# Optimization experiments

Hardware: AMD Instinct MI355X
Metric: run time of the kernel (lower is better)

## Reference

```python
import jax, jax.numpy as jnp
import numpy as np

N, E, IN_D, H, OUT_D = 50000, 800000, 128, 64, 64


def setup_inputs() -> dict:
    key = jax.random.key(0)
    ks = jax.random.split(key, 16)
    s = lambda k, shape: jax.random.normal(k, shape, dtype=jnp.float32) * (1.0 / np.sqrt(shape[0]))
    return {
        "x": jax.random.normal(ks[0], (N, IN_D), dtype=jnp.float32),
        "edge_index": jax.random.randint(ks[1], (2, E), 0, N, dtype=jnp.int32),
        "W1": s(ks[2], (IN_D, H)), "b1": jnp.zeros((H,), jnp.float32),
        "W2": s(ks[3], (H, 2 * H)), "b2": jnp.zeros((2 * H,), jnp.float32),
        "W3": s(ks[4], (2 * H, 4 * H)), "b3": jnp.zeros((4 * H,), jnp.float32),
        "dec1_w": s(ks[5], (4 * H, 2 * H, 2)), "dec1_b": jnp.zeros((2 * H,), jnp.float32),
        "dec2_w": s(ks[6], (2 * H, H, 2)), "dec2_b": jnp.zeros((H,), jnp.float32),
        "dec3_w": s(ks[7], (H, H, 2)), "dec3_b": jnp.zeros((H,), jnp.float32),
        "skip1_w": s(ks[8], (2 * H, 2 * H)), "skip1_b": jnp.zeros((2 * H,), jnp.float32),
        "skip2_w": s(ks[9], (H, H)), "skip2_b": jnp.zeros((H,), jnp.float32),
        "fin_w": s(ks[10], (OUT_D, 8 * H)), "fin_b": jnp.zeros((OUT_D,), jnp.float32),
    }


def _deconv2(x, w, b):
    # ConvTranspose1d(kernel=2, stride=2): [n,c,l] x [c,o,2] -> [n,o,2l]
    y = jnp.einsum('ncl,cok->nolk', x, w)
    n, o = x.shape[0], w.shape[1]
    return y.reshape(n, o, -1) + b[None, :, None]


def reference(x, edge_index, W1, b1, W2, b2, W3, b3, dec1_w, dec1_b, dec2_w, dec2_b,
              dec3_w, dec3_b, skip1_w, skip1_b, skip2_w, skip2_b, fin_w, fin_b):
    n = x.shape[0]
    loop = jnp.arange(n, dtype=edge_index.dtype)
    src = jnp.concatenate([edge_index[0], loop])
    tgt = jnp.concatenate([edge_index[1], loop])
    deg = jax.ops.segment_sum(jnp.ones_like(src, dtype=x.dtype), tgt, num_segments=n)
    dinv = jax.lax.rsqrt(deg)  # deg >= 1 due to self-loops
    norm = dinv[src] * dinv[tgt]  # [E+N]

    def gcn(h, W, b):
        hw = h @ W
        agg = jax.ops.segment_sum(hw[src] * norm[:, None], tgt, num_segments=n)
        return agg + b

    x1 = jax.nn.gelu(gcn(x, W1, b1))    # [N, H]
    x2 = jax.nn.gelu(gcn(x1, W2, b2))   # [N, 2H]
    x3 = jax.nn.gelu(gcn(x2, W3, b3))   # [N, 4H]

    d = _deconv2(x3[:, :, None], dec1_w, dec1_b)           # [N, 2H, 2]
    d = d + (x2 @ skip1_w.T + skip1_b)[:, :, None]
    d = _deconv2(d, dec2_w, dec2_b)                        # [N, H, 4]
    d = d + (x1 @ skip2_w.T + skip2_b)[:, :, None]
    d = _deconv2(d, dec3_w, dec3_b)                        # [N, H, 8]
    out = d.reshape(n, -1) @ fin_w.T + fin_b               # [N, OUT_D]
    return out
```

## Files before the change

### kernel.cpp

```cpp
#include <hip/hip_runtime.h>
#include <hip/hip_bf16.h>

typedef __attribute__((ext_vector_type(8))) short short8_t;
typedef __attribute__((ext_vector_type(4))) float f32x4;

#define CAP 64

__device__ __forceinline__ float gelu_f(float x) {
    float x3 = x * x * x;
    return 0.5f * x * (1.0f + tanhf(0.7978845608028654f * (x + 0.044715f * x3)));
}
__device__ __forceinline__ float b2f(unsigned short u) {
    union { float f; unsigned int i; } c; c.i = ((unsigned int)u) << 16; return c.f;
}
__device__ __forceinline__ unsigned short f2bu(float f) {
    union { float f; unsigned int i; } c; c.f = f;
    unsigned int r = c.i + 0x7fffu + ((c.i >> 16) & 1u);
    return (unsigned short)(r >> 16);
}


__device__ __forceinline__ void d_EF(int bid, int t, const float* __restrict__ dec3_w,
                                     const float* __restrict__ fin_w, float* __restrict__ EF) {
    int i2 = bid * 4 + (t >> 6), od = t & 63;
    int c3 = i2 >> 2, pp = i2 & 3;
    const float* d3 = dec3_w + c3 * 128;
    const float* fw = fin_w + od * 512;
    float s = 0.f;
    #pragma unroll
    for (int o3 = 0; o3 < 64; ++o3) {
        s += d3[o3 * 2 + 0] * fw[o3 * 8 + pp * 2 + 0];
        s += d3[o3 * 2 + 1] * fw[o3 * 8 + pp * 2 + 1];
    }
    EF[i2 * 64 + od] = s;
}

__device__ __forceinline__ void d_CEF(int bid, int t, const float* __restrict__ dec2_w,
                                      const float* __restrict__ EF, float* __restrict__ CEF) {
    int i1 = bid * 4 + (t >> 6), od = t & 63;
    int c2 = i1 >> 1, lp = i1 & 1;
    const float* d2 = dec2_w + c2 * 128;
    float s = 0.f;
    #pragma unroll
    for (int o2 = 0; o2 < 64; ++o2) {
        s += d2[o2 * 2 + 0] * EF[(o2 * 4 + lp * 2 + 0) * 64 + od];
        s += d2[o2 * 2 + 1] * EF[(o2 * 4 + lp * 2 + 1) * 64 + od];
    }
    CEF[i1 * 64 + od] = s;
}

__device__ __forceinline__ void d_comp(int sb, int od,
                       const float* __restrict__ dec1_w, const float* __restrict__ skip1_w,
                       const float* __restrict__ skip2_w,
                       const float* __restrict__ dec1_b, const float* __restrict__ skip1_b,
                       const float* __restrict__ dec2_b, const float* __restrict__ skip2_b,
                       const float* __restrict__ dec3_b, const float* __restrict__ fin_w,
                       const float* __restrict__ fin_b,
                       const float* __restrict__ CEF, const float* __restrict__ EF,
                       unsigned short* __restrict__ McatT, float* __restrict__ m0) {
    if (sb < 256) {
        const float* d1 = dec1_w + sb * 256;
        float s = 0.f;
        for (int j = 0; j < 256; ++j) s += d1[j] * CEF[j * 64 + od];
        McatT[od * 448 + sb] = f2bu(s);
    } else if (sb < 384) {
        int c = sb - 256;
        float s = 0.f;
        for (int j = 0; j < 256; ++j) s += skip1_w[(j >> 1) * 128 + c] * CEF[j * 64 + od];
        McatT[od * 448 + sb] = f2bu(s);
    } else if (sb < 448) {
        int c = sb - 384;
        float s = 0.f;
        for (int j = 0; j < 256; ++j) s += skip2_w[(j >> 2) * 64 + c] * EF[j * 64 + od];
        McatT[od * 448 + sb] = f2bu(s);
    } else {
        float s = fin_b[od];
        for (int j = 0; j < 256; ++j) s += (dec1_b[j >> 1] + skip1_b[j >> 1]) * CEF[j * 64 + od];
        for (int j = 0; j < 256; ++j) s += (dec2_b[j >> 2] + skip2_b[j >> 2]) * EF[j * 64 + od];
        for (int j = 0; j < 512; ++j) s += dec3_b[j >> 3] * fin_w[od * 512 + j];
        m0[od] = s;
    }
}

__device__ __forceinline__ void d_wconv(int bid, int t,
                        const float* __restrict__ W1, const float* __restrict__ W2,
                        const float* __restrict__ W3,
                        unsigned short* __restrict__ W1T, unsigned short* __restrict__ W2T,
                        unsigned short* __restrict__ W3T) {
    int i = bid * 256 + t;
    if (i < 8192) {
        int k = i >> 6, n = i & 63;
        W1T[n * 128 + k] = f2bu(W1[i]);
    } else if (i < 16384) {
        int j = i - 8192; int k = j >> 7, n = j & 127;
        W2T[n * 64 + k] = f2bu(W2[j]);
    } else if (i < 49152) {
        int j = i - 16384; int k = j >> 8, n = j & 255;
        W3T[n * 128 + k] = f2bu(W3[j]);
    }
}

__device__ __forceinline__ void d_fillx(int bid, int t, const int* __restrict__ src,
                                        const int* __restrict__ tgt, int E,
                                        int* __restrict__ cnt, int* __restrict__ csr) {
    int i = (bid * 256 + t) * 8;
    if (i + 7 < E) {
        int4 t0 = *(const int4*)(tgt + i);
        int4 t1 = *(const int4*)(tgt + i + 4);
        int4 s0 = *(const int4*)(src + i);
        int4 s1 = *(const int4*)(src + i + 4);
        int k0 = atomicAdd(&cnt[t0.x], 1);
        int k1 = atomicAdd(&cnt[t0.y], 1);
        int k2 = atomicAdd(&cnt[t0.z], 1);
        int k3 = atomicAdd(&cnt[t0.w], 1);
        int k4 = atomicAdd(&cnt[t1.x], 1);
        int k5 = atomicAdd(&cnt[t1.y], 1);
        int k6 = atomicAdd(&cnt[t1.z], 1);
        int k7 = atomicAdd(&cnt[t1.w], 1);
        if (k0 < CAP) csr[(t0.x << 6) + k0] = s0.x;
        if (k1 < CAP) csr[(t0.y << 6) + k1] = s0.y;
        if (k2 < CAP) csr[(t0.z << 6) + k2] = s0.z;
        if (k3 < CAP) csr[(t0.w << 6) + k3] = s0.w;
        if (k4 < CAP) csr[(t1.x << 6) + k4] = s1.x;
        if (k5 < CAP) csr[(t1.y << 6) + k5] = s1.y;
        if (k6 < CAP) csr[(t1.z << 6) + k6] = s1.z;
        if (k7 < CAP) csr[(t1.w << 6) + k7] = s1.w;
    } else {
        for (int k = i; k < E; ++k) {
            int tt = tgt[k];
            int kk = atomicAdd(&cnt[tt], 1);
            if (kk < CAP) csr[(tt << 6) + kk] = src[k];
        }
    }
}

template<bool A32, bool BIAS, bool GELU, bool OUT32>
__device__ __forceinline__ void d_gmm(
    int bx, int by,
    const unsigned short* __restrict__ A, const float* __restrict__ Af, int lda,
    const unsigned short* __restrict__ Bt,
    const float* __restrict__ bias,
    void* __restrict__ Cv, int ldc, int M, int K) {
    constexpr int LDS_R = 72;
    __shared__ unsigned short As[64 * LDS_R];
    __shared__ unsigned short Bs[64 * LDS_R];
    const int tid = threadIdx.x;
    const int r0 = bx * 64, c0 = by * 64;
    const int w = tid >> 6, lane = tid & 63;
    const int wm = (w >> 1) * 32, wn = (w & 1) * 32;
    const int fr = lane & 15, kg = lane >> 4;
    f32x4 acc[2][2];
    #pragma unroll
    for (int m = 0; m < 2; ++m)
        #pragma unroll
        for (int n = 0; n < 2; ++n) { f32x4 z = {0.f, 0.f, 0.f, 0.f}; acc[m][n] = z; }

    const int sr = tid >> 2, sc = (tid & 3) * 16;
    const bool aok = (r0 + sr) < M;
    const unsigned short* ag = A32 ? nullptr : (A + (size_t)(r0 + sr) * lda + sc);
    const float* agf = A32 ? (Af + (size_t)(r0 + sr) * lda + sc) : nullptr;
    const unsigned short* bg = Bt + (size_t)(c0 + sr) * K + sc;

    for (int kt = 0; kt < K; kt += 64) {
        if (aok) {
            if constexpr (A32) {
                float4 f0 = *(const float4*)(agf + kt);
                float4 f1 = *(const float4*)(agf + kt + 4);
                float4 f2 = *(const float4*)(agf + kt + 8);
                float4 f3 = *(const float4*)(agf + kt + 12);
                unsigned short o[16] = { f2bu(f0.x), f2bu(f0.y), f2bu(f0.z), f2bu(f0.w),
                                         f2bu(f1.x), f2bu(f1.y), f2bu(f1.z), f2bu(f1.w),
                                         f2bu(f2.x), f2bu(f2.y), f2bu(f2.z), f2bu(f2.w),
                                         f2bu(f3.x), f2bu(f3.y), f2bu(f3.z), f2bu(f3.w) };
                *(uint4*)&As[sr * LDS_R + sc]     = ((const uint4*)o)[0];
                *(uint4*)&As[sr * LDS_R + sc + 8] = ((const uint4*)o)[1];
            } else {
                *(uint4*)&As[sr * LDS_R + sc]     = *(const uint4*)(ag + kt);
                *(uint4*)&As[sr * LDS_R + sc + 8] = *(const uint4*)(ag + kt + 8);
            }
        }
        *(uint4*)&Bs[sr * LDS_R + sc]     = *(const uint4*)(bg + kt);
        *(uint4*)&Bs[sr * LDS_R + sc + 8] = *(const uint4*)(bg + kt + 8);
        __syncthreads();
        #pragma unroll
        for (int s2 = 0; s2 < 2; ++s2) {
            short8_t afr[2], bfr[2];
            #pragma unroll
            for (int n = 0; n < 2; ++n)
                bfr[n] = *(const short8_t*)&Bs[(wn + n * 16 + fr) * LDS_R + s2 * 32 + kg * 8];
            #pragma unroll
            for (int m = 0; m < 2; ++m)
                afr[m] = *(const short8_t*)&As[(wm + m * 16 + fr) * LDS_R + s2 * 32 + kg * 8];
            #pragma unroll
            for (int m = 0; m < 2; ++m)
                #pragma unroll
                for (int n = 0; n < 2; ++n)
                    acc[m][n] = __builtin_amdgcn_mfma_f32_16x16x32_bf16(afr[m], bfr[n], acc[m][n], 0, 0, 0);
        }
        __syncthreads();
    }
    #pragma unroll
    for (int m = 0; m < 2; ++m) {
        #pragma unroll
        for (int n = 0; n < 2; ++n) {
            #pragma unroll
            for (int j = 0; j < 4; ++j) {
                int row = r0 + wm + m * 16 + kg * 4 + j;
                int col = c0 + wn + n * 16 + fr;
                if (row < M) {
                    float xv = acc[m][n][j];
                    if (BIAS) xv += bias[col];
                    if (GELU) xv = gelu_f(xv);
                    if (OUT32) ((float*)Cv)[(size_t)row * ldc + col] = xv;
                    else ((unsigned short*)Cv)[(size_t)row * ldc + col] = f2bu(xv);
                }
            }
        }
    }
}

template<int F, int LPN, bool EPI>
__device__ __forceinline__ void d_aggb(
    int bid,
    const unsigned short* __restrict__ g, int ldi,
    const int* __restrict__ cnt, const int* __restrict__ csr,
    const float* __restrict__ bias,
    unsigned short* __restrict__ out, int ldo, int N) {
    constexpr int SLOTS = 64 / LPN;
    static_assert(F / LPN == 8, "V must be 8");
    __shared__ int   sIdx[4][CAP];
    __shared__ float sW[4][CAP];
    int tid = threadIdx.x;
    int lane = tid & 63, wv = tid >> 6;
    int v = bid * 4 + wv;
    bool ok = v < N;
    int vc = ok ? v : 0;
    int slot = lane / LPN, fl = lane % LPN;
    int fo = fl * 8;
    int deg = cnt[vc];
    float dv = rsqrtf((float)(deg + 1));
    int degc = min(deg, CAP);
    int u_l = (lane < degc) ? csr[(vc << 6) + lane] : vc;
    sIdx[wv][lane] = u_l;
    sW[wv][lane] = rsqrtf((float)(cnt[u_l] + 1)) * dv;
    __syncthreads();
    if (!ok) return;
    int cntE = degc + 1;
    float acc[8] = {};
    const unsigned short* hbase = g + fo;
    int j = slot;
    for (; j + SLOTS < cntE; j += 2 * SLOTS) {
        int s0 = (j > 0) ? (j - 1) : 0;
        int u0 = (j == 0) ? v : sIdx[wv][s0];
        float w0 = (j == 0) ? dv * dv : sW[wv][s0];
        int u1 = sIdx[wv][j + SLOTS - 1];
        float w1 = sW[wv][j + SLOTS - 1];
        uint4 t0 = *(const uint4*)(hbase + (size_t)u0 * ldi);
        uint4 t1 = *(const uint4*)(hbase + (size_t)u1 * ldi);
        const unsigned short* a0 = (const unsigned short*)&t0;
        const unsigned short* a1 = (const unsigned short*)&t1;
        #pragma unroll
        for (int q = 0; q < 8; ++q) acc[q] = fmaf(b2f(a0[q]), w0, acc[q]);
        #pragma unroll
        for (int q = 0; q < 8; ++q) acc[q] = fmaf(b2f(a1[q]), w1, acc[q]);
    }
    if (j < cntE) {
        int s0 = (j > 0) ? (j - 1) : 0;
        int u = (j == 0) ? v : sIdx[wv][s0];
        float wgt = (j == 0) ? dv * dv : sW[wv][s0];
        uint4 t = *(const uint4*)(hbase + (size_t)u * ldi);
        const unsigned short* ts = (const unsigned short*)&t;
        #pragma unroll
        for (int q = 0; q < 8; ++q) acc[q] = fmaf(b2f(ts[q]), wgt, acc[q]);
    }
    #pragma unroll
    for (int off = LPN; off < 64; off <<= 1)
        #pragma unroll
        for (int q = 0; q < 8; ++q) acc[q] += __shfl_xor(acc[q], off, 64);
    if (slot == 0) {
        unsigned short o[8];
        #pragma unroll
        for (int q = 0; q < 8; ++q) {
            float xv = acc[q];
            if (EPI) xv = gelu_f(xv + bias[fo + q]);
            o[q] = f2bu(xv);
        }
        *(uint4*)(out + (size_t)v * ldo + fo) = *(const uint4*)o;
    }
}


template<bool A32, bool BIAS, bool GELU, bool OUT32>
__global__ __launch_bounds__(256) void k_gmm(
    const unsigned short* __restrict__ A, const float* __restrict__ Af, int lda,
    const unsigned short* __restrict__ Bt,
    const float* __restrict__ bias,
    void* __restrict__ Cv, int ldc, int M, int K) {
    d_gmm<A32, BIAS, GELU, OUT32>(blockIdx.x, blockIdx.y, A, Af, lda, Bt, bias, Cv, ldc, M, K);
}

template<int F, int LPN, bool EPI>
__global__ __launch_bounds__(256) void k_aggb(
    const unsigned short* __restrict__ g, int ldi,
    const int* __restrict__ cnt, const int* __restrict__ csr,
    const float* __restrict__ bias,
    unsigned short* __restrict__ out, int ldo, int N) {
    d_aggb<F, LPN, EPI>(blockIdx.x, g, ldi, cnt, csr, bias, out, ldo, N);
}

__global__ __launch_bounds__(256) void k_mega0(
    const float* __restrict__ W1, const float* __restrict__ W2, const float* __restrict__ W3,
    unsigned short* __restrict__ W1T, unsigned short* __restrict__ W2T,
    unsigned short* __restrict__ W3T,
    const float* __restrict__ dec3_w, const float* __restrict__ fin_w, float* __restrict__ EF,
    int* __restrict__ cnt, int N) {
    int b = blockIdx.x, t = threadIdx.x;
    if (b < 192) d_wconv(b, t, W1, W2, W3, W1T, W2T, W3T);
    else if (b < 256) d_EF(b - 192, t, dec3_w, fin_w, EF);
    else { int i = (b - 256) * 256 + t; if (i < N) cnt[i] = 0; }
}

__global__ __launch_bounds__(256) void k_megaA(
    const int* __restrict__ src, const int* __restrict__ tgt, int E,
    int* __restrict__ cnt, int* __restrict__ csr, int nf,
    const float* __restrict__ x, const unsigned short* __restrict__ W1T,
    unsigned short* __restrict__ hw1, int M, int ng,
    const float* __restrict__ dec2_w, const float* __restrict__ EF, float* __restrict__ CEF) {
    int b = blockIdx.x;
    if (b < nf)
        d_fillx(b, threadIdx.x, src, tgt, E, cnt, csr);
    else if (b < nf + ng)
        d_gmm<true, false, false, false>(b - nf, 0, nullptr, x, 128, W1T,
                                         (const float*)nullptr, hw1, 64, M, 128);
    else
        d_CEF(b - nf - ng, threadIdx.x, dec2_w, EF, CEF);
}

__global__ __launch_bounds__(256) void k_megaB(
    const unsigned short* __restrict__ hw1,
    const int* __restrict__ cnt, const int* __restrict__ csr,
    const float* __restrict__ b1, unsigned short* __restrict__ x1out, int N, int na,
    const float* __restrict__ dec1_w, const float* __restrict__ skip1_w,
    const float* __restrict__ skip2_w,
    const float* __restrict__ dec1_b, const float* __restrict__ skip1_b,
    const float* __restrict__ dec2_b, const float* __restrict__ skip2_b,
    const float* __restrict__ dec3_b, const float* __restrict__ fin_w,
    const float* __restrict__ fin_b,
    const float* __restrict__ CEF, const float* __restrict__ EF,
    unsigned short* __restrict__ McatT, float* __restrict__ m0) {
    int b = blockIdx.x, t = threadIdx.x;
    if (b < na) {
        d_aggb<64, 8, true>(b, hw1, 64, cnt, csr, b1, x1out, 448, N);
    } else {
        int sb = (b - na) * 4 + (t >> 6);
        if (sb <= 448)
            d_comp(sb, t & 63, dec1_w, skip1_w, skip2_w, dec1_b, skip1_b, dec2_b, skip2_b,
                   dec3_b, fin_w, fin_b, CEF, EF, McatT, m0);
    }
}

extern "C" void kernel_launch(void* const* d_in, const int* in_sizes, int n_in,
                              void* d_out, int out_size, void* d_ws, size_t ws_size,
                              hipStream_t stream) {
    const float* x       = (const float*)d_in[0];
    const int*   ei      = (const int*)d_in[1];
    const float* W1      = (const float*)d_in[2];
    const float* b1      = (const float*)d_in[3];
    const float* W2      = (const float*)d_in[4];
    const float* b2      = (const float*)d_in[5];
    const float* W3      = (const float*)d_in[6];
    const float* b3      = (const float*)d_in[7];
    const float* dec1_w  = (const float*)d_in[8];
    const float* dec1_b  = (const float*)d_in[9];
    const float* dec2_w  = (const float*)d_in[10];
    const float* dec2_b  = (const float*)d_in[11];
    const float* dec3_w  = (const float*)d_in[12];
    const float* dec3_b  = (const float*)d_in[13];
    const float* skip1_w = (const float*)d_in[14];
    const float* skip1_b = (const float*)d_in[15];
    const float* skip2_w = (const float*)d_in[16];
    const float* skip2_b = (const float*)d_in[17];
    const float* fin_w   = (const float*)d_in[18];
    const float* fin_b   = (const float*)d_in[19];

    const int N = in_sizes[0] / 128;
    const int E = in_sizes[1] / 2;
    const int* e_src = ei;
    const int* e_tgt = ei + E;

    char* p = (char*)d_ws;
    auto alloc = [&](size_t bytes) -> void* {
        void* r = p;
        p += (bytes + 255) & ~(size_t)255;
        return r;
    };
    int*   cnt     = (int*)alloc((size_t)N * 4);
    int*   csr     = (int*)alloc((size_t)N * CAP * 4);
    float* EF      = (float*)alloc(256 * 64 * 4);
    float* CEF     = (float*)alloc(256 * 64 * 4);
    float* m0      = (float*)alloc(64 * 4);
    unsigned short* McatT = (unsigned short*)alloc(64 * 448 * 2);
    unsigned short* W1T   = (unsigned short*)alloc(64 * 128 * 2);
    unsigned short* W2T   = (unsigned short*)alloc(128 * 64 * 2);
    unsigned short* W3T   = (unsigned short*)alloc(256 * 128 * 2);
    unsigned short* hw1   = (unsigned short*)alloc((size_t)N * 64 * 2);
    unsigned short* a1    = (unsigned short*)alloc((size_t)N * 64 * 2);
    unsigned short* xcat  = (unsigned short*)alloc((size_t)N * 448 * 2);
    unsigned short* a2    = hw1;
    if ((size_t)(p - (char*)d_ws) > ws_size) return;

    const int nf = (E / 8 + 255) / 256;
    const int mg = (N + 63) / 64;
    const int ag = (N + 3) / 4;
    const int compb = (449 + 3) / 4;
    const int zb = (N + 255) / 256;

    k_mega0<<<dim3(192 + 64 + zb), dim3(256), 0, stream>>>(
        W1, W2, W3, W1T, W2T, W3T, dec3_w, fin_w, EF, cnt, N);

    k_megaA<<<dim3(nf + mg + 64), dim3(256), 0, stream>>>(
        e_src, e_tgt, E, cnt, csr, nf, x, W1T, hw1, N, mg, dec2_w, EF, CEF);

    k_megaB<<<dim3(ag + compb), dim3(256), 0, stream>>>(
        hw1, cnt, csr, b1, xcat + 384, N, ag,
        dec1_w, skip1_w, skip2_w, dec1_b, skip1_b, dec2_b, skip2_b, dec3_b,
        fin_w, fin_b, CEF, EF, McatT, m0);

    k_aggb<64, 8, false><<<dim3(ag), dim3(256), 0, stream>>>(
        xcat + 384, 448, cnt, csr, (const float*)nullptr, a1, 64, N);
    k_gmm<false, true, true, false><<<dim3(mg, 2), dim3(256), 0, stream>>>(
        a1, nullptr, 64, W2T, b2, xcat + 256, 448, N, 64);

    k_aggb<128, 16, false><<<dim3(ag), dim3(256), 0, stream>>>(
        xcat + 256, 448, cnt, csr, (const float*)nullptr, a2, 128, N);
    k_gmm<false, true, true, false><<<dim3(mg, 4), dim3(256), 0, stream>>>(
        a2, nullptr, 128, W3T, b3, xcat, 448, N, 128);

    k_gmm<false, true, false, true><<<dim3(mg, 1), dim3(256), 0, stream>>>(
        xcat, nullptr, 448, McatT, m0, d_out, 64, N, 448);
}
```

Before: 213.9 us.

## Process two nodes per wavefront in GCN aggregation to raise memory parallelism

Each wavefront in the neighbor-aggregation routine now handles two destination nodes, interleaving four independent row gathers per iteration instead of two. The self-loop is folded into the shared-memory neighbor list, with zero-weight padding beyond the degree, which removes per-iteration branching. The intent is more gathers in flight per wave and half as many blocks. In exchange it uses more registers, does wasted zero-weight loads when the two nodes have unequal degrees, and lowers the neighbor cap by one.

New measurement: 203.3 us. 5.0% less time.

```diff
diff --git a/kernel.cpp b/kernel.cpp
--- a/kernel.cpp
+++ b/kernel.cpp
@@ -228,64 +228,94 @@
     unsigned short* __restrict__ out, int ldo, int N) {
     constexpr int SLOTS = 64 / LPN;
     static_assert(F / LPN == 8, "V must be 8");
-    __shared__ int   sIdx[4][CAP];
-    __shared__ float sW[4][CAP];
+    __shared__ int   sIdx[4][2][CAP];
+    __shared__ float sW[4][2][CAP];
     int tid = threadIdx.x;
     int lane = tid & 63, wv = tid >> 6;
-    int v = bid * 4 + wv;
-    bool ok = v < N;
-    int vc = ok ? v : 0;
+    int v0 = bid * 8 + wv * 2;
+    int v1 = v0 + 1;
+    bool ok0 = v0 < N, ok1 = v1 < N;
+    int vc0 = ok0 ? v0 : 0, vc1 = ok1 ? v1 : 0;
     int slot = lane / LPN, fl = lane % LPN;
     int fo = fl * 8;
-    int deg = cnt[vc];
-    float dv = rsqrtf((float)(deg + 1));
-    int degc = min(deg, CAP);
-    int u_l = (lane < degc) ? csr[(vc << 6) + lane] : vc;
-    sIdx[wv][lane] = u_l;
-    sW[wv][lane] = rsqrtf((float)(cnt[u_l] + 1)) * dv;
+    int deg0 = cnt[vc0], deg1 = cnt[vc1];
+    float dv0 = rsqrtf((float)(deg0 + 1)), dv1 = rsqrtf((float)(deg1 + 1));
+    int degc0 = min(deg0, CAP - 1), degc1 = min(deg1, CAP - 1);
+    int ua = (lane < degc0) ? csr[(vc0 << 6) + lane] : vc0;
+    int ub = (lane < degc1) ? csr[(vc1 << 6) + lane] : vc1;
+    int ca = cnt[ua], cb = cnt[ub];
+    float wa = (lane < degc0) ? rsqrtf((float)(ca + 1)) * dv0
+                              : ((lane == degc0) ? dv0 * dv0 : 0.f);
+    float wb = (lane < degc1) ? rsqrtf((float)(cb + 1)) * dv1
+                              : ((lane == degc1) ? dv1 * dv1 : 0.f);
+    sIdx[wv][0][lane] = ua;  sW[wv][0][lane] = wa;
+    sIdx[wv][1][lane] = ub;  sW[wv][1][lane] = wb;
     __syncthreads();
-    if (!ok) return;
-    int cntE = degc + 1;
-    float acc[8] = {};
+    int cntE0 = ok0 ? degc0 + 1 : 0;
+    int cntE1 = ok1 ? degc1 + 1 : 0;
+    int cmax = max(cntE0, cntE1);
+    float acc0[8] = {}, acc1[8] = {};
     const unsigned short* hbase = g + fo;
     int j = slot;
-    for (; j + SLOTS < cntE; j += 2 * SLOTS) {
-        int s0 = (j > 0) ? (j - 1) : 0;
-        int u0 = (j == 0) ? v : sIdx[wv][s0];
-        float w0 = (j == 0) ? dv * dv : sW[wv][s0];
-        int u1 = sIdx[wv][j + SLOTS - 1];
-        float w1 = sW[wv][j + SLOTS - 1];
+    for (; j + SLOTS < cmax; j += 2 * SLOTS) {
+        int u00 = sIdx[wv][0][j];          float w00 = sW[wv][0][j];
+        int u01 = sIdx[wv][0][j + SLOTS];  float w01 = sW[wv][0][j + SLOTS];
+        int u10 = sIdx[wv][1][j];          float w10 = sW[wv][1][j];
+        int u11 = sIdx[wv][1][j + SLOTS];  float w11 = sW[wv][1][j + SLOTS];
+        uint4 t00 = *(const uint4*)(hbase + (size_t)u00 * ldi);
+        uint4 t01 = *(const uint4*)(hbase + (size_t)u01 * ldi);
+        uint4 t10 = *(const uint4*)(hbase + (size_t)u10 * ldi);
+        uint4 t11 = *(const uint4*)(hbase + (size_t)u11 * ldi);
+        const unsigned short* p00 = (const unsigned short*)&t00;
+        const unsigned short* p01 = (const unsigned short*)&t01;
+        const unsigned short* p10 = (const unsigned short*)&t10;
+        const unsigned short* p11 = (const unsigned short*)&t11;
+        #pragma unroll
+        for (int q = 0; q < 8; ++q) {
+            acc0[q] = fmaf(b2f(p00[q]), w00, acc0[q]);
+            acc1[q] = fmaf(b2f(p10[q]), w10, acc1[q]);
+        }
+        #pragma unroll
+        for (int q = 0; q < 8; ++q) {
+            acc0[q] = fmaf(b2f(p01[q]), w01, acc0[q]);
+            acc1[q] = fmaf(b2f(p11[q]), w11, acc1[q]);
+        }
+    }
+    if (j < cmax) {
+        int u0 = sIdx[wv][0][j];  float w0 = sW[wv][0][j];
+        int u1 = sIdx[wv][1][j];  float w1 = sW[wv][1][j];
         uint4 t0 = *(const uint4*)(hbase + (size_t)u0 * ldi);
         uint4 t1 = *(const uint4*)(hbase + (size_t)u1 * ldi);
-        const unsigned short* a0 = (const unsigned short*)&t0;
-        const unsigned short* a1 = (const unsigned short*)&t1;
-        #pragma unroll
-        for (int q = 0; q < 8; ++q) acc[q] = fmaf(b2f(a0[q]), w0, acc[q]);
-        #pragma unroll
-        for (int q = 0; q < 8; ++q) acc[q] = fmaf(b2f(a1[q]), w1, acc[q]);
-    }
-    if (j < cntE) {
-        int s0 = (j > 0) ? (j - 1) : 0;
-        int u = (j == 0) ? v : sIdx[wv][s0];
-        float wgt = (j == 0) ? dv * dv : sW[wv][s0];
-        uint4 t = *(const uint4*)(hbase + (size_t)u * ldi);
-        const unsigned short* ts = (const unsigned short*)&t;
-        #pragma unroll
-        for (int q = 0; q < 8; ++q) acc[q] = fmaf(b2f(ts[q]), wgt, acc[q]);
+        const unsigned short* p0 = (const unsigned short*)&t0;
+        const unsigned short* p1 = (const unsigned short*)&t1;
+        #pragma unroll
+        for (int q = 0; q < 8; ++q) {
+            acc0[q] = fmaf(b2f(p0[q]), w0, acc0[q]);
+            acc1[q] = fmaf(b2f(p1[q]), w1, acc1[q]);
+        }
     }
     #pragma unroll
     for (int off = LPN; off < 64; off <<= 1)
         #pragma unroll
-        for (int q = 0; q < 8; ++q) acc[q] += __shfl_xor(acc[q], off, 64);
+        for (int q = 0; q < 8; ++q) {
+            acc0[q] += __shfl_xor(acc0[q], off, 64);
+            acc1[q] += __shfl_xor(acc1[q], off, 64);
+        }
     if (slot == 0) {
-        unsigned short o[8];
+        unsigned short o0[8], o1[8];
         #pragma unroll
         for (int q = 0; q < 8; ++q) {
-            float xv = acc[q];
-            if (EPI) xv = gelu_f(xv + bias[fo + q]);
-            o[q] = f2bu(xv);
-        }
-        *(uint4*)(out + (size_t)v * ldo + fo) = *(const uint4*)o;
+            float x0 = acc0[q], x1 = acc1[q];
+            if (EPI) {
+                float bq = bias[fo + q];
+                x0 = gelu_f(x0 + bq);
+                x1 = gelu_f(x1 + bq);
+            }
+            o0[q] = f2bu(x0);
+            o1[q] = f2bu(x1);
+        }
+        if (ok0) *(uint4*)(out + (size_t)v0 * ldo + fo) = *(const uint4*)o0;
+        if (ok1) *(uint4*)(out + (size_t)v1 * ldo + fo) = *(const uint4*)o1;
     }
 }
 
@@ -411,7 +441,7 @@
 
     const int nf = (E / 8 + 255) / 256;
     const int mg = (N + 63) / 64;
-    const int ag = (N + 3) / 4;
+    const int ag = (N + 7) / 8;
     const int compb = (449 + 3) / 4;
     const int zb = (N + 255) / 256;
 
```
